# Performance work log

Hardware: AMD Instinct MI355X
Metric: run time of the kernel (lower is better)

Reference implementation:

```python
import jax, jax.numpy as jnp
import numpy as np

LN_EPS = 1e-6
IGNORE_INDEX = -100

D_MODEL = 768
VOCAB = 32128
B, S = 4, 512


def setup_inputs() -> dict:
    key = jax.random.key(0)
    k1, k2, k3 = jax.random.split(key, 3)
    hidden_states = jax.random.normal(k1, (B, S, D_MODEL), dtype=jnp.float32)
    labels = jax.random.randint(k2, (B, S), 0, VOCAB, dtype=jnp.int64)
    ln_weight = jnp.ones((D_MODEL,), dtype=jnp.float32)
    # nn.Linear(d_model, vocab, bias=False).weight has shape [vocab, d_model]
    lm_head_weight = jax.random.normal(k3, (VOCAB, D_MODEL), dtype=jnp.float32) * (D_MODEL ** -0.5)
    return {
        "hidden_states": hidden_states,
        "labels": labels,
        "ln_weight": ln_weight,
        "lm_head_weight": lm_head_weight,
    }


def t5_layer_norm(x, weight, eps=LN_EPS):
    # T5-style RMSNorm: no mean subtraction, variance in fp32
    variance = jnp.mean(x.astype(jnp.float32) ** 2, axis=-1, keepdims=True)
    x = x * jax.lax.rsqrt(variance + eps)
    return weight * x


def reference(hidden_states, labels, ln_weight, lm_head_weight):
    h = t5_layer_norm(hidden_states, ln_weight)
    # dropout is identity in eval / rate=0
    # lm_head: [B,S,D] @ [V,D]^T -> [B,S,V]
    prediction_scores = jnp.einsum("bsd,vd->bsv", h, lm_head_weight)
    # CrossEntropyLoss(ignore_index=-100), mean over non-ignored tokens
    logits = prediction_scores.reshape(-1, VOCAB)  # [B*S, V]
    flat_labels = labels.reshape(-1)
    valid = flat_labels != IGNORE_INDEX
    safe_labels = jnp.where(valid, flat_labels, 0)
    logp = jax.nn.log_softmax(logits, axis=-1)
    nll = -jnp.take_along_axis(logp, safe_labels[:, None], axis=-1)[:, 0]
    nll = jnp.where(valid, nll, 0.0)
    loss = jnp.sum(nll) / jnp.maximum(jnp.sum(valid.astype(jnp.float32)), 1.0)
    return (loss, prediction_scores)
```

## Files before the change

### kernel.cpp

```cpp
#include <hip/hip_runtime.h>
#include <stdint.h>

#define DM 768
#define VOC 32128
#define NTOK 2048
#define NBY (VOC / 128)
#define IGN (-100)

typedef __bf16 bf16x8 __attribute__((ext_vector_type(8)));
typedef float f32x4 __attribute__((ext_vector_type(4)));

typedef __attribute__((address_space(1))) void gvoid_t;
typedef __attribute__((address_space(3))) void svoid_t;

__device__ __forceinline__ void gl_lds16(const void* g, void* s) {
  __builtin_amdgcn_global_load_lds((gvoid_t*)g, (svoid_t*)s, 16, 0, 0);
}

__device__ __forceinline__ unsigned short f2bf(float f) {
  unsigned int u = __float_as_uint(f);
  u = (u + 0x7fffu + ((u >> 16) & 1u)) >> 16;
  return (unsigned short)u;
}

__global__ void __launch_bounds__(256) cvt_w_kernel(const float* __restrict__ W,
                                                    unsigned short* __restrict__ Wb) {
  size_t i = ((size_t)blockIdx.x * 256 + threadIdx.x) * 4;
  float4 v = *(const float4*)(W + i);
  ushort4 o;
  o.x = f2bf(v.x); o.y = f2bf(v.y); o.z = f2bf(v.z); o.w = f2bf(v.w);
  *(ushort4*)(Wb + i) = o;
}

__global__ void __launch_bounds__(256) rmsnorm_kernel(const float* __restrict__ x,
                                                      const float* __restrict__ w,
                                                      unsigned short* __restrict__ h) {
  int tok = blockIdx.x;
  const float* xr = x + (size_t)tok * DM;
  int t = threadIdx.x;
  float v0 = xr[t], v1 = xr[t + 256], v2 = xr[t + 512];
  float ss = v0 * v0 + v1 * v1 + v2 * v2;
  for (int off = 32; off; off >>= 1) ss += __shfl_down(ss, off);
  __shared__ float red[4];
  int wv = t >> 6, ln = t & 63;
  if (ln == 0) red[wv] = ss;
  __syncthreads();
  float tot = red[0] + red[1] + red[2] + red[3];
  float inv = rsqrtf(tot * (1.0f / DM) + 1e-6f);
  unsigned short* hr = h + (size_t)tok * DM;
  hr[t]       = f2bf(v0 * inv * w[t]);
  hr[t + 256] = f2bf(v1 * inv * w[t + 256]);
  hr[t + 512] = f2bf(v2 * inv * w[t + 512]);
}

#define TILE_ELEMS 24576
#define A_ELEMS    16384

__global__ void __launch_bounds__(512, 2) gemm_kernel(const unsigned short* __restrict__ A,
                                                      const unsigned short* __restrict__ Bw,
                                                      float* __restrict__ C,
                                                      float* __restrict__ Pm,
                                                      float* __restrict__ Ps) {
  __shared__ __align__(16) unsigned short LDS[3 * TILE_ELEMS];

  const int id = blockIdx.x;
  const int w  = (id & 7) * 251 + (id >> 3);
  const int by = w >> 3;
  const int m0 = (w & 7) * 256;
  const int n0 = by * 128;

  const int tid  = threadIdx.x;
  const int wv   = tid >> 6, ln = tid & 63;
  const int l15  = ln & 15, quad = ln >> 4;
  const int wvm  = wv >> 1;
  const int wvn  = wv & 1;

  const int lr  = ln >> 3;
  const int qsw = ((ln & 7) ^ lr) * 8;
  const unsigned short* aS = A  + (size_t)(m0 + wv * 32 + lr) * DM + qsw;
  const unsigned short* bS = Bw + (size_t)(n0 + wv * 16 + lr) * DM + qsw;
  const int aDof = wv * 32 * 64;
  const int bDof = A_ELEMS + wv * 16 * 64;

  auto STAGE = [&](unsigned short* sb, int kt) {
    const unsigned short* a = aS + kt * 64;
    const unsigned short* b = bS + kt * 64;
    unsigned short* ad = sb + aDof;
    unsigned short* bd = sb + bDof;
#pragma unroll
    for (int c = 0; c < 4; ++c) gl_lds16(a + (size_t)c * (8 * DM), ad + c * 512);
#pragma unroll
    for (int c = 0; c < 2; ++c) gl_lds16(b + (size_t)c * (8 * DM), bd + c * 512);
  };

  f32x4 acc[4][4];
#pragma unroll
  for (int i = 0; i < 4; ++i)
#pragma unroll
    for (int j = 0; j < 4; ++j) {
      acc[i][j][0] = 0.f; acc[i][j][1] = 0.f; acc[i][j][2] = 0.f; acc[i][j][3] = 0.f;
    }

  const int sw = l15 & 7;
  auto COMPUTE = [&](const unsigned short* At) {
    const unsigned short* Bt = At + A_ELEMS;
#pragma unroll
    for (int kk = 0; kk < 2; ++kk) {
      const int so = ((kk * 4 + quad) ^ sw) * 8;
      bf16x8 a[4], b[4];
#pragma unroll
      for (int i = 0; i < 4; ++i) {
        a[i] = *(const bf16x8*)(At + (wvm * 64 + i * 16 + l15) * 64 + so);
        b[i] = *(const bf16x8*)(Bt + (wvn * 64 + i * 16 + l15) * 64 + so);
      }
      __builtin_amdgcn_s_setprio(1);
#pragma unroll
      for (int mi = 0; mi < 4; ++mi)
#pragma unroll
        for (int ni = 0; ni < 4; ++ni)
          acc[mi][ni] = __builtin_amdgcn_mfma_f32_16x16x32_bf16(a[mi], b[ni], acc[mi][ni], 0, 0, 0);
      __builtin_amdgcn_s_setprio(0);
    }
  };

  unsigned short* p0 = LDS;
  unsigned short* p1 = LDS + TILE_ELEMS;
  unsigned short* p2 = LDS + 2 * TILE_ELEMS;

  STAGE(p0, 0);
  STAGE(p1, 1);
  asm volatile("s_waitcnt vmcnt(6)" ::: "memory");
  __builtin_amdgcn_s_barrier();

  for (int t = 0; t < 10; ++t) {
    STAGE(p2, t + 2);
    COMPUTE(p0);
    asm volatile("s_waitcnt vmcnt(6)" ::: "memory");
    __builtin_amdgcn_s_barrier();
    unsigned short* tmp = p0; p0 = p1; p1 = p2; p2 = tmp;
  }
  COMPUTE(p0);
  asm volatile("s_waitcnt vmcnt(0)" ::: "memory");
  __builtin_amdgcn_s_barrier();
  COMPUTE(p1);

#pragma unroll
  for (int mi = 0; mi < 4; ++mi) {
#pragma unroll
    for (int r = 0; r < 4; ++r) {
      const int row = m0 + wvm * 64 + mi * 16 + quad * 4 + r;
      float* cp = C + (size_t)row * VOC + (n0 + wvn * 64 + l15);
#pragma unroll
      for (int ni = 0; ni < 4; ++ni)
        __builtin_nontemporal_store(acc[mi][ni][r], cp + ni * 16);
    }
  }

  float* pmL = (float*)LDS;
  float* psL = pmL + 512;
  float rm[4][4], rs[4][4];
#pragma unroll
  for (int mi = 0; mi < 4; ++mi) {
#pragma unroll
    for (int r = 0; r < 4; ++r) {
      float m = fmaxf(fmaxf(acc[mi][0][r], acc[mi][1][r]),
                      fmaxf(acc[mi][2][r], acc[mi][3][r]));
#pragma unroll
      for (int off = 1; off < 16; off <<= 1) m = fmaxf(m, __shfl_xor(m, off));
      float s = __expf(acc[mi][0][r] - m) + __expf(acc[mi][1][r] - m) +
                __expf(acc[mi][2][r] - m) + __expf(acc[mi][3][r] - m);
#pragma unroll
      for (int off = 1; off < 16; off <<= 1) s += __shfl_xor(s, off);
      rm[mi][r] = m; rs[mi][r] = s;
    }
  }
  if (l15 == 0) {
#pragma unroll
    for (int mi = 0; mi < 4; ++mi)
#pragma unroll
      for (int r = 0; r < 4; ++r) {
        int rr = wvm * 64 + mi * 16 + quad * 4 + r;
        pmL[wvn * 256 + rr] = rm[mi][r];
        psL[wvn * 256 + rr] = rs[mi][r];
      }
  }
  __syncthreads();
  if (tid < 256) {
    float ma = pmL[tid], mb = pmL[256 + tid];
    float nm = fmaxf(ma, mb);
    float S = psL[tid] * __expf(ma - nm) + psL[256 + tid] * __expf(mb - nm);
    Pm[(size_t)by * NTOK + m0 + tid] = nm;
    Ps[(size_t)by * NTOK + m0 + tid] = S;
  }
}

__global__ void __launch_bounds__(256) loss_finalize_kernel(const float* __restrict__ Pm,
                                                            const float* __restrict__ Ps,
                                                            const float* __restrict__ scores,
                                                            const int* __restrict__ labels,
                                                            float* __restrict__ nll) {
  const int tok = blockIdx.x;
  float m = -1e30f, s = 0.f;
  for (int j = threadIdx.x; j < NBY; j += 256) {
    float m2 = Pm[(size_t)j * NTOK + tok], s2 = Ps[(size_t)j * NTOK + tok];
    float nm = fmaxf(m, m2);
    s = s * __expf(m - nm) + s2 * __expf(m2 - nm);
    m = nm;
  }
  for (int off = 32; off; off >>= 1) {
    float m2 = __shfl_down(m, off), s2 = __shfl_down(s, off);
    float nm = fmaxf(m, m2);
    s = s * __expf(m - nm) + s2 * __expf(m2 - nm);
    m = nm;
  }
  __shared__ float ms[4], sh[4];
  int wv = threadIdx.x >> 6, ln = threadIdx.x & 63;
  if (ln == 0) { ms[wv] = m; sh[wv] = s; }
  __syncthreads();
  if (threadIdx.x == 0) {
    float M = ms[0], S = sh[0];
    for (int i = 1; i < 4; ++i) {
      float nm = fmaxf(M, ms[i]);
      S = S * __expf(M - nm) + sh[i] * __expf(ms[i] - nm);
      M = nm;
    }
    int lab = labels[tok];
    float v = 0.f;
    if (lab != IGN) v = (M + logf(S)) - scores[(size_t)tok * VOC + lab];
    nll[tok] = v;
  }
}

__global__ void __launch_bounds__(256) reduce_kernel(const float* __restrict__ nll,
                                                     const int* __restrict__ labels,
                                                     float* __restrict__ out) {
  float s = 0.f, c = 0.f;
  for (int i = threadIdx.x; i < NTOK; i += 256) {
    s += nll[i];
    c += (labels[i] != IGN) ? 1.0f : 0.0f;
  }
  for (int off = 32; off; off >>= 1) { s += __shfl_down(s, off); c += __shfl_down(c, off); }
  __shared__ float rs[4], rc[4];
  int wv = threadIdx.x >> 6, ln = threadIdx.x & 63;
  if (ln == 0) { rs[wv] = s; rc[wv] = c; }
  __syncthreads();
  if (threadIdx.x == 0) {
    float S = rs[0] + rs[1] + rs[2] + rs[3];
    float Cc = rc[0] + rc[1] + rc[2] + rc[3];
    out[0] = S / fmaxf(Cc, 1.0f);
  }
}

extern "C" void kernel_launch(void* const* d_in, const int* in_sizes, int n_in,
                              void* d_out, int out_size, void* d_ws, size_t ws_size,
                              hipStream_t stream) {
  const float* hs     = (const float*)d_in[0];
  const int*   labels = (const int*)d_in[1];
  const float* lnw    = (const float*)d_in[2];
  const float* W      = (const float*)d_in[3];

  float* out    = (float*)d_out;
  float* scores = out + 1;

  char* ws = (char*)d_ws;
  unsigned short* Wb = (unsigned short*)ws;                 ws += (size_t)VOC * DM * 2;
  unsigned short* Hb = (unsigned short*)ws;                 ws += (size_t)NTOK * DM * 2;
  float* Pm          = (float*)ws;                          ws += (size_t)NBY * NTOK * 4;
  float* Ps          = (float*)ws;                          ws += (size_t)NBY * NTOK * 4;
  float* nll         = (float*)ws;

  cvt_w_kernel<<<(VOC * DM / 4) / 256, 256, 0, stream>>>(W, Wb);
  rmsnorm_kernel<<<NTOK, 256, 0, stream>>>(hs, lnw, Hb);
  gemm_kernel<<<8 * NBY, 512, 0, stream>>>(Hb, Wb, scores, Pm, Ps);
  loss_finalize_kernel<<<NTOK, 256, 0, stream>>>(Pm, Ps, scores, labels, nll);
  reduce_kernel<<<1, 256, 0, stream>>>(nll, labels, out);
}
```

Before: 473.1 us.

## Interleave half-tile global loads with MFMA phases using extra barriers

Splits each K-tile's async global-to-LDS staging into two halves, issued between the LDS fragment reads and the MFMA block of each half-K step. Barriers and lgkmcnt waits are added around each MFMA cluster, in a ping-pong style schedule. The aim is to spread memory issue across compute and keep waves in lockstep so loads overlap with matrix math. The cost is four barriers per K-tile instead of one, which may add sync overhead. A barrier is also added before the LDS reuse in the epilogue.

Result: slower. 483.2 us (+2.2%).

```diff
diff --git a/kernel.cpp b/kernel.cpp
--- a/kernel.cpp
+++ b/kernel.cpp
@@ -82,15 +82,20 @@
   const int aDof = wv * 32 * 64;
   const int bDof = A_ELEMS + wv * 16 * 64;
 
-  auto STAGE = [&](unsigned short* sb, int kt) {
+  auto STAGE_H = [&](unsigned short* sb, int kt, int h) {
     const unsigned short* a = aS + kt * 64;
     const unsigned short* b = bS + kt * 64;
     unsigned short* ad = sb + aDof;
     unsigned short* bd = sb + bDof;
-#pragma unroll
-    for (int c = 0; c < 4; ++c) gl_lds16(a + (size_t)c * (8 * DM), ad + c * 512);
-#pragma unroll
-    for (int c = 0; c < 2; ++c) gl_lds16(b + (size_t)c * (8 * DM), bd + c * 512);
+    if (h == 0) {
+      gl_lds16(a, ad);
+      gl_lds16(a + (size_t)8 * DM, ad + 512);
+      gl_lds16(b, bd);
+    } else {
+      gl_lds16(a + (size_t)16 * DM, ad + 1024);
+      gl_lds16(a + (size_t)24 * DM, ad + 1536);
+      gl_lds16(b + (size_t)8 * DM, bd + 512);
+    }
   };
 
   f32x4 acc[4][4];
@@ -102,17 +107,28 @@
     }
 
   const int sw = l15 & 7;
-  auto COMPUTE = [&](const unsigned short* At) {
-    const unsigned short* Bt = At + A_ELEMS;
-#pragma unroll
-    for (int kk = 0; kk < 2; ++kk) {
-      const int so = ((kk * 4 + quad) ^ sw) * 8;
+
+  unsigned short* p0 = LDS;
+  unsigned short* p1 = LDS + TILE_ELEMS;
+  unsigned short* p2 = LDS + 2 * TILE_ELEMS;
+
+  STAGE_H(p0, 0, 0); STAGE_H(p0, 0, 1);
+  STAGE_H(p1, 1, 0); STAGE_H(p1, 1, 1);
+  asm volatile("s_waitcnt vmcnt(6)" ::: "memory");
+  __builtin_amdgcn_s_barrier();
+
+  for (int t = 0; t < 12; ++t) {
+    {
+      const int so = (quad ^ sw) * 8;
       bf16x8 a[4], b[4];
 #pragma unroll
       for (int i = 0; i < 4; ++i) {
-        a[i] = *(const bf16x8*)(At + (wvm * 64 + i * 16 + l15) * 64 + so);
-        b[i] = *(const bf16x8*)(Bt + (wvn * 64 + i * 16 + l15) * 64 + so);
+        a[i] = *(const bf16x8*)(p0 + (wvm * 64 + i * 16 + l15) * 64 + so);
+        b[i] = *(const bf16x8*)(p0 + A_ELEMS + (wvn * 64 + i * 16 + l15) * 64 + so);
       }
+      if (t < 10) STAGE_H(p2, t + 2, 0);
+      __builtin_amdgcn_s_barrier();
+      asm volatile("s_waitcnt lgkmcnt(0)" ::: "memory");
       __builtin_amdgcn_s_setprio(1);
 #pragma unroll
       for (int mi = 0; mi < 4; ++mi)
@@ -120,29 +136,35 @@
         for (int ni = 0; ni < 4; ++ni)
           acc[mi][ni] = __builtin_amdgcn_mfma_f32_16x16x32_bf16(a[mi], b[ni], acc[mi][ni], 0, 0, 0);
       __builtin_amdgcn_s_setprio(0);
-    }
-  };
-
-  unsigned short* p0 = LDS;
-  unsigned short* p1 = LDS + TILE_ELEMS;
-  unsigned short* p2 = LDS + 2 * TILE_ELEMS;
-
-  STAGE(p0, 0);
-  STAGE(p1, 1);
-  asm volatile("s_waitcnt vmcnt(6)" ::: "memory");
-  __builtin_amdgcn_s_barrier();
-
-  for (int t = 0; t < 10; ++t) {
-    STAGE(p2, t + 2);
-    COMPUTE(p0);
-    asm volatile("s_waitcnt vmcnt(6)" ::: "memory");
-    __builtin_amdgcn_s_barrier();
+      __builtin_amdgcn_s_barrier();
+    }
+    {
+      const int so = ((4 + quad) ^ sw) * 8;
+      bf16x8 a[4], b[4];
+#pragma unroll
+      for (int i = 0; i < 4; ++i) {
+        a[i] = *(const bf16x8*)(p0 + (wvm * 64 + i * 16 + l15) * 64 + so);
+        b[i] = *(const bf16x8*)(p0 + A_ELEMS + (wvn * 64 + i * 16 + l15) * 64 + so);
+      }
+      if (t < 10) {
+        STAGE_H(p2, t + 2, 1);
+        asm volatile("s_waitcnt vmcnt(6)" ::: "memory");
+      } else if (t == 10) {
+        asm volatile("s_waitcnt vmcnt(0)" ::: "memory");
+      }
+      __builtin_amdgcn_s_barrier();
+      asm volatile("s_waitcnt lgkmcnt(0)" ::: "memory");
+      __builtin_amdgcn_s_setprio(1);
+#pragma unroll
+      for (int mi = 0; mi < 4; ++mi)
+#pragma unroll
+        for (int ni = 0; ni < 4; ++ni)
+          acc[mi][ni] = __builtin_amdgcn_mfma_f32_16x16x32_bf16(a[mi], b[ni], acc[mi][ni], 0, 0, 0);
+      __builtin_amdgcn_s_setprio(0);
+      __builtin_amdgcn_s_barrier();
+    }
     unsigned short* tmp = p0; p0 = p1; p1 = p2; p2 = tmp;
   }
-  COMPUTE(p0);
-  asm volatile("s_waitcnt vmcnt(0)" ::: "memory");
-  __builtin_amdgcn_s_barrier();
-  COMPUTE(p1);
 
 #pragma unroll
   for (int mi = 0; mi < 4; ++mi) {
@@ -174,6 +196,7 @@
       rm[mi][r] = m; rs[mi][r] = s;
     }
   }
+  __builtin_amdgcn_s_barrier();
   if (l15 == 0) {
 #pragma unroll
     for (int mi = 0; mi < 4; ++mi)
```

## Enlarge GEMM tile to 256x256 with padded vocab and double-buffered LDS

Applied to the files above, without the earlier changes.

The GEMM block tile grows from 256x128 to 256x256, so each wave computes a 128x64 sub-tile with 32 accumulators. The vocab is padded to 32256 with zero bf16 rows, and edge columns are masked in the store and softmax-partial code. Triple buffering becomes double buffering, with fine-grained barriers interleaving LDS fragment loads and MFMA groups. The aim is to halve A-operand reloads per FLOP and raise arithmetic intensity per LDS byte, at the cost of more accumulator registers, extra barriers and a little wasted compute on padding.

New measurement: 516.9 us. +9.3%, slower.

```diff
diff --git a/kernel.cpp b/kernel.cpp
--- a/kernel.cpp
+++ b/kernel.cpp
@@ -3,8 +3,9 @@
 
 #define DM 768
 #define VOC 32128
+#define VOCP 32256
 #define NTOK 2048
-#define NBY (VOC / 128)
+#define NBY2 126
 #define IGN (-100)
 
 typedef __bf16 bf16x8 __attribute__((ext_vector_type(8)));
@@ -23,12 +24,19 @@
   return (unsigned short)u;
 }
 
+#define BAR()   asm volatile("s_barrier" ::: "memory")
+#define LGKM0() asm volatile("s_waitcnt lgkmcnt(0)" ::: "memory")
+
 __global__ void __launch_bounds__(256) cvt_w_kernel(const float* __restrict__ W,
                                                     unsigned short* __restrict__ Wb) {
   size_t i = ((size_t)blockIdx.x * 256 + threadIdx.x) * 4;
-  float4 v = *(const float4*)(W + i);
   ushort4 o;
-  o.x = f2bf(v.x); o.y = f2bf(v.y); o.z = f2bf(v.z); o.w = f2bf(v.w);
+  if (i < (size_t)VOC * DM) {
+    float4 v = *(const float4*)(W + i);
+    o.x = f2bf(v.x); o.y = f2bf(v.y); o.z = f2bf(v.z); o.w = f2bf(v.w);
+  } else {
+    o.x = 0; o.y = 0; o.z = 0; o.w = 0;
+  }
   *(ushort4*)(Wb + i) = o;
 }
 
@@ -53,34 +61,35 @@
   hr[t + 512] = f2bf(v2 * inv * w[t + 512]);
 }
 
-#define TILE_ELEMS 24576
-#define A_ELEMS    16384
+#define BUF_ELEMS 32768
+#define B_OFF     16384
 
 __global__ void __launch_bounds__(512, 2) gemm_kernel(const unsigned short* __restrict__ A,
                                                       const unsigned short* __restrict__ Bw,
                                                       float* __restrict__ C,
                                                       float* __restrict__ Pm,
                                                       float* __restrict__ Ps) {
-  __shared__ __align__(16) unsigned short LDS[3 * TILE_ELEMS];
-
-  const int id = blockIdx.x;
-  const int w  = (id & 7) * 251 + (id >> 3);
-  const int by = w >> 3;
-  const int m0 = (w & 7) * 256;
-  const int n0 = by * 128;
+  __shared__ __align__(16) unsigned short LDS[2 * BUF_ELEMS];
+
+  const int id  = blockIdx.x;
+  const int w   = (id & 7) * 126 + (id >> 3);
+  const int nt  = w >> 3;
+  const int m0  = (w & 7) * 256;
+  const int n0  = nt * 256;
 
   const int tid  = threadIdx.x;
   const int wv   = tid >> 6, ln = tid & 63;
   const int l15  = ln & 15, quad = ln >> 4;
-  const int wvm  = wv >> 1;
-  const int wvn  = wv & 1;
+  const int wvm  = wv >> 2;
+  const int wvn  = wv & 3;
+  const int sw   = l15 & 7;
 
   const int lr  = ln >> 3;
   const int qsw = ((ln & 7) ^ lr) * 8;
   const unsigned short* aS = A  + (size_t)(m0 + wv * 32 + lr) * DM + qsw;
-  const unsigned short* bS = Bw + (size_t)(n0 + wv * 16 + lr) * DM + qsw;
+  const unsigned short* bS = Bw + (size_t)(n0 + wv * 32 + lr) * DM + qsw;
   const int aDof = wv * 32 * 64;
-  const int bDof = A_ELEMS + wv * 16 * 64;
+  const int bDof = B_OFF + wv * 32 * 64;
 
   auto STAGE = [&](unsigned short* sb, int kt) {
     const unsigned short* a = aS + kt * 64;
@@ -88,109 +97,139 @@
     unsigned short* ad = sb + aDof;
     unsigned short* bd = sb + bDof;
 #pragma unroll
-    for (int c = 0; c < 4; ++c) gl_lds16(a + (size_t)c * (8 * DM), ad + c * 512);
-#pragma unroll
-    for (int c = 0; c < 2; ++c) gl_lds16(b + (size_t)c * (8 * DM), bd + c * 512);
+    for (int c = 0; c < 4; ++c) {
+      gl_lds16(a + (size_t)c * (8 * DM), ad + c * 512);
+      gl_lds16(b + (size_t)c * (8 * DM), bd + c * 512);
+    }
   };
 
-  f32x4 acc[4][4];
-#pragma unroll
-  for (int i = 0; i < 4; ++i)
+  f32x4 acc[8][4];
+#pragma unroll
+  for (int i = 0; i < 8; ++i)
 #pragma unroll
     for (int j = 0; j < 4; ++j) {
       acc[i][j][0] = 0.f; acc[i][j][1] = 0.f; acc[i][j][2] = 0.f; acc[i][j][3] = 0.f;
     }
 
-  const int sw = l15 & 7;
-  auto COMPUTE = [&](const unsigned short* At) {
-    const unsigned short* Bt = At + A_ELEMS;
-#pragma unroll
-    for (int kk = 0; kk < 2; ++kk) {
-      const int so = ((kk * 4 + quad) ^ sw) * 8;
-      bf16x8 a[4], b[4];
-#pragma unroll
-      for (int i = 0; i < 4; ++i) {
-        a[i] = *(const bf16x8*)(At + (wvm * 64 + i * 16 + l15) * 64 + so);
-        b[i] = *(const bf16x8*)(Bt + (wvn * 64 + i * 16 + l15) * 64 + so);
+  bf16x8 a[4], b[4];
+  auto LDA4 = [&](const unsigned short* Ap, int mibase, int kk) {
+    const int so = (((kk << 2) + quad) ^ sw) * 8;
+#pragma unroll
+    for (int i = 0; i < 4; ++i)
+      a[i] = *(const bf16x8*)(Ap + (wvm * 128 + (mibase + i) * 16 + l15) * 64 + so);
+  };
+  auto LDB4 = [&](const unsigned short* Bp, int kk) {
+    const int so = (((kk << 2) + quad) ^ sw) * 8;
+#pragma unroll
+    for (int i = 0; i < 4; ++i)
+      b[i] = *(const bf16x8*)(Bp + (wvn * 64 + i * 16 + l15) * 64 + so);
+  };
+  auto MM16 = [&](int mibase) {
+    __builtin_amdgcn_s_setprio(1);
+#pragma unroll
+    for (int i = 0; i < 4; ++i)
+#pragma unroll
+      for (int j = 0; j < 4; ++j)
+        acc[mibase + i][j] =
+            __builtin_amdgcn_mfma_f32_16x16x32_bf16(a[i], b[j], acc[mibase + i][j], 0, 0, 0);
+    __builtin_amdgcn_s_setprio(0);
+  };
+
+  unsigned short* pc = LDS;
+  unsigned short* po = LDS + BUF_ELEMS;
+
+  STAGE(pc, 0); STAGE(po, 1);
+  asm volatile("s_waitcnt vmcnt(8)" ::: "memory");
+  BAR();
+
+  for (int t = 0; t < 12; ++t) {
+    const unsigned short* Ap = pc;
+    const unsigned short* Bp = pc + B_OFF;
+    LDB4(Bp, 0); LDA4(Ap, 0, 0);
+    LGKM0(); BAR();
+    MM16(0);
+    BAR();
+    LDA4(Ap, 4, 0);
+    LGKM0(); BAR();
+    MM16(4);
+    BAR();
+    LDB4(Bp, 1); LDA4(Ap, 0, 1);
+    LGKM0(); BAR();
+    MM16(0);
+    BAR();
+    LDA4(Ap, 4, 1);
+    LGKM0(); BAR();
+    if (t <= 9) STAGE(pc, t + 2);
+    MM16(4);
+    if (t <= 9)       { asm volatile("s_waitcnt vmcnt(8)" ::: "memory"); }
+    else if (t == 10) { asm volatile("s_waitcnt vmcnt(0)" ::: "memory"); }
+    BAR();
+    unsigned short* tmp = pc; pc = po; po = tmp;
+  }
+
+  bool vn[4];
+#pragma unroll
+  for (int ni = 0; ni < 4; ++ni) vn[ni] = (n0 + wvn * 64 + ni * 16) < VOC;
+
+  if (n0 + 256 <= VOC) {
+#pragma unroll
+    for (int mi = 0; mi < 8; ++mi) {
+#pragma unroll
+      for (int r = 0; r < 4; ++r) {
+        const int row = m0 + wvm * 128 + mi * 16 + quad * 4 + r;
+        float* cp = C + (size_t)row * VOC + (n0 + wvn * 64 + l15);
+#pragma unroll
+        for (int ni = 0; ni < 4; ++ni)
+          __builtin_nontemporal_store(acc[mi][ni][r], cp + ni * 16);
       }
-      __builtin_amdgcn_s_setprio(1);
-#pragma unroll
-      for (int mi = 0; mi < 4; ++mi)
+    }
+  } else {
+#pragma unroll
+    for (int mi = 0; mi < 8; ++mi) {
+#pragma unroll
+      for (int r = 0; r < 4; ++r) {
+        const int row = m0 + wvm * 128 + mi * 16 + quad * 4 + r;
+        float* cp = C + (size_t)row * VOC + (n0 + wvn * 64 + l15);
 #pragma unroll
         for (int ni = 0; ni < 4; ++ni)
-          acc[mi][ni] = __builtin_amdgcn_mfma_f32_16x16x32_bf16(a[mi], b[ni], acc[mi][ni], 0, 0, 0);
-      __builtin_amdgcn_s_setprio(0);
-    }
-  };
-
-  unsigned short* p0 = LDS;
-  unsigned short* p1 = LDS + TILE_ELEMS;
-  unsigned short* p2 = LDS + 2 * TILE_ELEMS;
-
-  STAGE(p0, 0);
-  STAGE(p1, 1);
-  asm volatile("s_waitcnt vmcnt(6)" ::: "memory");
-  __builtin_amdgcn_s_barrier();
-
-  for (int t = 0; t < 10; ++t) {
-    STAGE(p2, t + 2);
-    COMPUTE(p0);
-    asm volatile("s_waitcnt vmcnt(6)" ::: "memory");
-    __builtin_amdgcn_s_barrier();
-    unsigned short* tmp = p0; p0 = p1; p1 = p2; p2 = tmp;
-  }
-  COMPUTE(p0);
-  asm volatile("s_waitcnt vmcnt(0)" ::: "memory");
-  __builtin_amdgcn_s_barrier();
-  COMPUTE(p1);
-
-#pragma unroll
-  for (int mi = 0; mi < 4; ++mi) {
+          if (vn[ni]) __builtin_nontemporal_store(acc[mi][ni][r], cp + ni * 16);
+      }
+    }
+  }
+
+  float* pmL = (float*)LDS;
+  float* psL = pmL + 1024;
+#pragma unroll
+  for (int mi = 0; mi < 8; ++mi) {
 #pragma unroll
     for (int r = 0; r < 4; ++r) {
-      const int row = m0 + wvm * 64 + mi * 16 + quad * 4 + r;
-      float* cp = C + (size_t)row * VOC + (n0 + wvn * 64 + l15);
+      float m = -3.0e38f;
 #pragma unroll
       for (int ni = 0; ni < 4; ++ni)
-        __builtin_nontemporal_store(acc[mi][ni][r], cp + ni * 16);
-    }
-  }
-
-  float* pmL = (float*)LDS;
-  float* psL = pmL + 512;
-  float rm[4][4], rs[4][4];
-#pragma unroll
-  for (int mi = 0; mi < 4; ++mi) {
-#pragma unroll
-    for (int r = 0; r < 4; ++r) {
-      float m = fmaxf(fmaxf(acc[mi][0][r], acc[mi][1][r]),
-                      fmaxf(acc[mi][2][r], acc[mi][3][r]));
+        if (vn[ni]) m = fmaxf(m, acc[mi][ni][r]);
 #pragma unroll
       for (int off = 1; off < 16; off <<= 1) m = fmaxf(m, __shfl_xor(m, off));
-      float s = __expf(acc[mi][0][r] - m) + __expf(acc[mi][1][r] - m) +
-                __expf(acc[mi][2][r] - m) + __expf(acc[mi][3][r] - m);
+      float s = 0.f;
+#pragma unroll
+      for (int ni = 0; ni < 4; ++ni)
+        if (vn[ni]) s += __expf(acc[mi][ni][r] - m);
 #pragma unroll
       for (int off = 1; off < 16; off <<= 1) s += __shfl_xor(s, off);
-      rm[mi][r] = m; rs[mi][r] = s;
-    }
-  }
-  if (l15 == 0) {
-#pragma unroll
-    for (int mi = 0; mi < 4; ++mi)
-#pragma unroll
-      for (int r = 0; r < 4; ++r) {
-        int rr = wvm * 64 + mi * 16 + quad * 4 + r;
-        pmL[wvn * 256 + rr] = rm[mi][r];
-        psL[wvn * 256 + rr] = rs[mi][r];
+      if (l15 == 0) {
+        int rr = wvm * 128 + mi * 16 + quad * 4 + r;
+        pmL[wvn * 256 + rr] = m;
+        psL[wvn * 256 + rr] = s;
       }
-  }
-  __syncthreads();
+    }
+  }
+  LGKM0(); BAR();
   if (tid < 256) {
-    float ma = pmL[tid], mb = pmL[256 + tid];
-    float nm = fmaxf(ma, mb);
-    float S = psL[tid] * __expf(ma - nm) + psL[256 + tid] * __expf(mb - nm);
-    Pm[(size_t)by * NTOK + m0 + tid] = nm;
-    Ps[(size_t)by * NTOK + m0 + tid] = S;
+    float ma = pmL[tid], mb = pmL[256 + tid], mc = pmL[512 + tid], md = pmL[768 + tid];
+    float M = fmaxf(fmaxf(ma, mb), fmaxf(mc, md));
+    float S = psL[tid] * __expf(ma - M) + psL[256 + tid] * __expf(mb - M) +
+              psL[512 + tid] * __expf(mc - M) + psL[768 + tid] * __expf(md - M);
+    Pm[(size_t)nt * NTOK + m0 + tid] = M;
+    Ps[(size_t)nt * NTOK + m0 + tid] = S;
   }
 }
 
@@ -201,7 +240,7 @@
                                                             float* __restrict__ nll) {
   const int tok = blockIdx.x;
   float m = -1e30f, s = 0.f;
-  for (int j = threadIdx.x; j < NBY; j += 256) {
+  for (int j = threadIdx.x; j < NBY2; j += 256) {
     float m2 = Pm[(size_t)j * NTOK + tok], s2 = Ps[(size_t)j * NTOK + tok];
     float nm = fmaxf(m, m2);
     s = s * __expf(m - nm) + s2 * __expf(m2 - nm);
@@ -263,15 +302,15 @@
   float* scores = out + 1;
 
   char* ws = (char*)d_ws;
-  unsigned short* Wb = (unsigned short*)ws;                 ws += (size_t)VOC * DM * 2;
+  unsigned short* Wb = (unsigned short*)ws;                 ws += (size_t)VOCP * DM * 2;
   unsigned short* Hb = (unsigned short*)ws;                 ws += (size_t)NTOK * DM * 2;
-  float* Pm          = (float*)ws;                          ws += (size_t)NBY * NTOK * 4;
-  float* Ps          = (float*)ws;                          ws += (size_t)NBY * NTOK * 4;
+  float* Pm          = (float*)ws;                          ws += (size_t)NBY2 * NTOK * 4;
+  float* Ps          = (float*)ws;                          ws += (size_t)NBY2 * NTOK * 4;
   float* nll         = (float*)ws;
 
-  cvt_w_kernel<<<(VOC * DM / 4) / 256, 256, 0, stream>>>(W, Wb);
+  cvt_w_kernel<<<(VOCP * DM / 4) / 256, 256, 0, stream>>>(W, Wb);
   rmsnorm_kernel<<<NTOK, 256, 0, stream>>>(hs, lnw, Hb);
-  gemm_kernel<<<8 * NBY, 512, 0, stream>>>(Hb, Wb, scores, Pm, Ps);
+  gemm_kernel<<<8 * NBY2, 512, 0, stream>>>(Hb, Wb, scores, Pm, Ps);
   loss_finalize_kernel<<<NTOK, 256, 0, stream>>>(Pm, Ps, scores, labels, nll);
   reduce_kernel<<<1, 256, 0, stream>>>(nll, labels, out);
 }
```
